# Kernel tuning notes

Measured on AMD Instinct MI355X. Metric: run time of the kernel, lower is better.

## Reference

```python
import jax, jax.numpy as jnp
import numpy as np

B, T, N = 32, 512, 16
C, V, D, H, L = 150, 832, 512, 512, 5  # chord vocab, note vocab, embed dim, hidden, layers


def setup_inputs() -> dict:
    key = jax.random.key(0)
    ks = jax.random.split(key, 16)
    s = 0.05
    note = jax.random.randint(ks[0], (B, T, N), 0, V)
    chord = jax.random.randint(ks[1], (B, T), 0, C)
    chord_table = jax.random.normal(ks[2], (C, D), jnp.float32) * s
    note_table = jax.random.normal(ks[3], (V, D), jnp.float32) * s
    # GRU layer 0 (input = 2*D), layers 1..L-1 (input = H), gate order r,z,n like torch
    w_ih0 = jax.random.normal(ks[4], (3 * H, 2 * D), jnp.float32) * s
    w_hh0 = jax.random.normal(ks[5], (3 * H, H), jnp.float32) * s
    b_ih0 = jax.random.normal(ks[6], (3 * H,), jnp.float32) * s
    b_hh0 = jax.random.normal(ks[7], (3 * H,), jnp.float32) * s
    w_ih_r = jax.random.normal(ks[8], (L - 1, 3 * H, H), jnp.float32) * s
    w_hh_r = jax.random.normal(ks[9], (L - 1, 3 * H, H), jnp.float32) * s
    b_ih_r = jax.random.normal(ks[10], (L - 1, 3 * H), jnp.float32) * s
    b_hh_r = jax.random.normal(ks[11], (L - 1, 3 * H), jnp.float32) * s
    fc_w = jax.random.normal(ks[12], (C, H), jnp.float32) * s
    fc_b = jax.random.normal(ks[13], (C,), jnp.float32) * s
    return dict(note=note, chord=chord, chord_table=chord_table, note_table=note_table,
                w_ih0=w_ih0, w_hh0=w_hh0, b_ih0=b_ih0, b_hh0=b_hh0,
                w_ih_r=w_ih_r, w_hh_r=w_hh_r, b_ih_r=b_ih_r, b_hh_r=b_hh_r,
                fc_w=fc_w, fc_b=fc_b)


def _gru_layer(x, wih, whh, bih, bhh):
    # x: [B, T, in] -> [B, T, H], torch GRU cell math (gate order r,z,n)
    xp = jnp.einsum('bti,gi->btg', x, wih) + bih          # precompute input proj [B,T,3H]
    xp = jnp.swapaxes(xp, 0, 1)                            # [T,B,3H]
    h0 = jnp.zeros((x.shape[0], whh.shape[1]), x.dtype)

    def step(h, xpt):
        gh = h @ whh.T + bhh
        xr, xz, xn = jnp.split(xpt, 3, axis=-1)
        hr, hz, hn = jnp.split(gh, 3, axis=-1)
        r = jax.nn.sigmoid(xr + hr)
        z = jax.nn.sigmoid(xz + hz)
        n = jnp.tanh(xn + r * hn)
        h_new = (1.0 - z) * n + z * h
        return h_new, h_new

    _, ys = jax.lax.scan(step, h0, xp)
    return jnp.swapaxes(ys, 0, 1)                          # [B,T,H]


def _forward(note, chord, chord_table, note_table, w_ih0, w_hh0, b_ih0, b_hh0,
             w_ih_r, w_hh_r, b_ih_r, b_hh_r, fc_w, fc_b):
    # padding_idx=0: zero row 0 of both tables (also blocks its gradient)
    ct = chord_table.at[0].set(0.0)
    nt = note_table.at[0].set(0.0)
    chord_emb = ct[chord]                                   # [B,T,D]
    # ragged mean over notes before first zero; mask[k]=1 iff no zero in note[...,:k+1]
    mask = jnp.cumprod((note != 0).astype(chord_table.dtype), axis=-1)  # [B,T,N]
    emb = nt[note]                                          # [B,T,N,D]
    cnt = jnp.maximum(mask.sum(-1), 1.0)                    # zero_index==0 case -> mean of zero row
    note_emb = jnp.einsum('btnd,btn->btd', emb, mask) / cnt[..., None]
    x = jnp.concatenate([chord_emb, note_emb], axis=-1)     # [B,T,2D]
    x = _gru_layer(x, w_ih0, w_hh0, b_ih0, b_hh0)
    for l in range(w_ih_r.shape[0]):
        x = _gru_layer(x, w_ih_r[l], w_hh_r[l], b_ih_r[l], b_hh_r[l])
    return x @ fc_w.T + fc_b                                # [B,T,C]


def reference(note, chord, chord_table, note_table, w_ih0, w_hh0, b_ih0, b_hh0,
              w_ih_r, w_hh_r, b_ih_r, b_hh_r, fc_w, fc_b):
    return _forward(note, chord, chord_table, note_table, w_ih0, w_hh0, b_ih0, b_hh0,
                    w_ih_r, w_hh_r, b_ih_r, b_hh_r, fc_w, fc_b)
```

## Files before the change

kernel.cpp:

```cpp
#include <hip/hip_runtime.h>
#include <hip/hip_bf16.h>

#define B_   32
#define T_   512
#define NN_  16
#define CV_  150
#define D_   512
#define H_   512
#define BT_  16384
#define K0_  1024
#define G3H_ 1536
#define SUBS_ 32
#define NBF_ 160
#define WSZ_ 49152

using bf16x8 = __attribute__((ext_vector_type(8))) short;
using f32x4  = __attribute__((ext_vector_type(4))) float;
using u32x4  = __attribute__((ext_vector_type(4))) unsigned int;
typedef unsigned long long u64;

__device__ __forceinline__ unsigned short f2bf(float f){
  unsigned int u = __builtin_bit_cast(unsigned int, f);
  u += 0x7fffu + ((u >> 16) & 1u);
  return (unsigned short)(u >> 16);
}

__device__ __forceinline__ void store8(unsigned short* p, f32x4 a, f32x4 b){
  union { unsigned short us[8]; u32x4 v; } u;
  u.us[0]=f2bf(a[0]); u.us[1]=f2bf(a[1]); u.us[2]=f2bf(a[2]); u.us[3]=f2bf(a[3]);
  u.us[4]=f2bf(b[0]); u.us[5]=f2bf(b[1]); u.us[6]=f2bf(b[2]); u.us[7]=f2bf(b[3]);
  *(u32x4*)p = u.v;
}

__device__ __forceinline__ u64 ld_coh_u64(const u64* p){
  return __hip_atomic_load(p, __ATOMIC_RELAXED, __HIP_MEMORY_SCOPE_AGENT);
}
__device__ __forceinline__ void st_coh_u32(void* p, unsigned int v){
  __hip_atomic_store((unsigned int*)p, v, __ATOMIC_RELAXED, __HIP_MEMORY_SCOPE_AGENT);
}
__device__ __forceinline__ void st_flag(int* p, int v){
  __hip_atomic_store(p, v, __ATOMIC_RELAXED, __HIP_MEMORY_SCOPE_AGENT);
}
__device__ __forceinline__ int ld_flag(const int* p){
  return __hip_atomic_load(p, __ATOMIC_RELAXED, __HIP_MEMORY_SCOPE_AGENT);
}

__global__ void convert_bf16(const float* __restrict__ src,
                             unsigned short* __restrict__ dst, int n){
  int i = blockIdx.x * 256 + threadIdx.x;
  if (i < n) dst[i] = f2bf(src[i]);
}

__global__ void prep_wfrag(const float* __restrict__ whh0,
                           const float* __restrict__ whhr,
                           const float* __restrict__ wihr,
                           unsigned short* __restrict__ wsw, int total){
  int idx = blockIdx.x * 256 + threadIdx.x;
  if (idx >= total) return;
  int pos = idx & 511;
  int lam = pos >> 3, e = pos & 7;
  int fr  = idx >> 9;
  int ks  = fr & 31;
  int g   = (fr >> 5) % 3;
  int blk = fr / 96;
  int sub = blk & 31, l = blk >> 5;
  int row = g * 512 + sub * 16 + (lam & 15);
  int k   = (ks & 15) * 32 + (lam >> 4) * 8 + e;
  float v;
  if (l == 0) v = (ks < 16) ? whh0[(size_t)row * H_ + k] : 0.f;
  else {
    const float* w = (ks < 16) ? (whhr + (size_t)(l - 1) * G3H_ * H_)
                               : (wihr + (size_t)(l - 1) * G3H_ * H_);
    v = w[(size_t)row * H_ + k];
  }
  wsw[idx] = f2bf(v);
}

__global__ void prep_bias(const float* __restrict__ bhh0,
                          const float* __restrict__ bihr,
                          const float* __restrict__ bhhr,
                          float* __restrict__ bias_sw, int total){
  int idx = blockIdx.x * 256 + threadIdx.x;
  if (idx >= total) return;
  int q = idx & 3, u = (idx >> 2) & 15, sub = (idx >> 6) & 31, l = idx >> 11;
  int j = sub * 16 + u;
  float v;
  if (l == 0){
    v = (q == 0) ? bhh0[j] : (q == 1) ? bhh0[512 + j] : (q == 2) ? 0.f : bhh0[1024 + j];
  } else {
    const float* bi = bihr + (size_t)(l - 1) * G3H_;
    const float* bh = bhhr + (size_t)(l - 1) * G3H_;
    v = (q == 0) ? bi[j] + bh[j]
      : (q == 1) ? bi[512 + j] + bh[512 + j]
      : (q == 2) ? bi[1024 + j] : bh[1024 + j];
  }
  bias_sw[idx] = v;
}

__global__ __launch_bounds__(64) void emb_kernel(
    const int* __restrict__ note, const int* __restrict__ chord,
    const float* __restrict__ ctab, const float* __restrict__ ntab,
    unsigned short* __restrict__ x0){
  const int bt = blockIdx.x;
  const int tid = threadIdx.x;
  __shared__ int sn[NN_];
  if (tid < NN_) sn[tid] = note[bt * NN_ + tid];
  __syncthreads();
  float alive = 1.f, cnt = 0.f;
  float msk[NN_];
  #pragma unroll
  for (int k = 0; k < NN_; ++k){ if (sn[k] == 0) alive = 0.f; msk[k] = alive; cnt += alive; }
  const float inv = 1.f / fmaxf(cnt, 1.f);
  const int ch = chord[bt];
  const int d0 = tid * 8;
  f32x4 c0 = {0.f,0.f,0.f,0.f}, c1 = {0.f,0.f,0.f,0.f};
  if (ch != 0){
    const float* cp = ctab + (size_t)ch * D_ + d0;
    c0 = *(const f32x4*)cp; c1 = *(const f32x4*)(cp + 4);
  }
  f32x4 s0 = {0.f,0.f,0.f,0.f}, s1 = {0.f,0.f,0.f,0.f};
  #pragma unroll
  for (int k = 0; k < NN_; ++k){
    if (msk[k] != 0.f){
      const float* np = ntab + (size_t)sn[k] * D_ + d0;
      s0 += *(const f32x4*)np;
      s1 += *(const f32x4*)(np + 4);
    }
  }
  s0 *= inv; s1 *= inv;
  unsigned short* o = x0 + (size_t)bt * K0_ + d0;
  store8(o, c0, c1);
  store8(o + D_, s0, s1);
}

__global__ __launch_bounds__(256) void gemm_bt(
    const unsigned short* __restrict__ X, const unsigned short* __restrict__ W,
    const float* __restrict__ bias, float* __restrict__ Y,
    int M, int N, int K, int wmode){
  const int lane = threadIdx.x & 63;
  const int wave = threadIdx.x >> 6;
  const int l15 = lane & 15, kq4 = lane >> 4;
  const int m_frag = blockIdx.y * 64 + wave * 16 + l15;
  const int n_base = blockIdx.x * 64;
  f32x4 acc[4] = {{0.f,0.f,0.f,0.f},{0.f,0.f,0.f,0.f},{0.f,0.f,0.f,0.f},{0.f,0.f,0.f,0.f}};
  const unsigned short* xptr = X + (size_t)m_frag * K + kq4 * 8;
  const unsigned short* wptr[4];
  #pragma unroll
  for (int i = 0; i < 4; ++i){
    int n = n_base + i * 16 + l15;
    if (n >= N) n = N - 1;
    wptr[i] = W + (size_t)n * K + kq4 * 8;
  }
  for (int k0 = 0; k0 < K; k0 += 32){
    bf16x8 a = *(const bf16x8*)(xptr + k0);
    #pragma unroll
    for (int i = 0; i < 4; ++i){
      bf16x8 b = *(const bf16x8*)(wptr[i] + k0);
      acc[i] = __builtin_amdgcn_mfma_f32_16x16x32_bf16(a, b, acc[i], 0, 0, 0);
    }
  }
  const int mrow = blockIdx.y * 64 + wave * 16 + kq4 * 4;
  #pragma unroll
  for (int i = 0; i < 4; ++i){
    int n = n_base + i * 16 + l15;
    if (n < N){
      float bv = bias[n];
      #pragma unroll
      for (int r = 0; r < 4; ++r){
        int m = mrow + r;
        float v = acc[i][r] + bv;
        if (wmode == 0) Y[(size_t)m * N + n] = v;
        else            Y[((size_t)(m & (T_-1)) * N + n) * B_ + (m >> 9)] = v;
      }
    }
  }
}

__global__ __launch_bounds__(256, 1) void gru_fused(
    const float* __restrict__ xp, const unsigned short* __restrict__ wsw,
    const float* __restrict__ bias_sw, unsigned short* __restrict__ hT,
    unsigned short* __restrict__ xT, unsigned short* __restrict__ xout,
    int* __restrict__ flags){
  __shared__ unsigned short w_s[96 * 512];
  __shared__ unsigned short stage_s[32 * 512];
  __shared__ float p_s[4][2][16][16];

  const int tid = threadIdx.x;
  const int blk = blockIdx.x;
  const int l   = blk >> 5;
  const int sub = blk & 31;
  const int lane = tid & 63, wave = tid >> 6;
  const int l15 = lane & 15, l4 = lane >> 4;
  const int myn = wave >> 1;
  const bool rzw = (wave & 1) == 0;

  {
    const u32x4* src = (const u32x4*)(wsw + (size_t)blk * WSZ_);
    u32x4* dst = (u32x4*)w_s;
    #pragma unroll
    for (int i = 0; i < 24; ++i) dst[tid + 256 * i] = src[tid + 256 * i];
  }

  const int cb = tid & 31;
  const int cj = (tid >> 5) * 2;
  const int jg = sub * 16 + cj;
  const float* bsp = bias_sw + blk * 64;
  const float br0 = bsp[cj*4+0],     bz0 = bsp[cj*4+1],     bx0 = bsp[cj*4+2],     bn0 = bsp[cj*4+3];
  const float br1 = bsp[(cj+1)*4+0], bz1 = bsp[(cj+1)*4+1], bx1 = bsp[(cj+1)*4+2], bn1 = bsp[(cj+1)*4+3];
  float hres0 = 0.f, hres1 = 0.f;

  unsigned short* hTl = hT + (size_t)l * (2 * 32 * 512);
  unsigned short* xTw = xT + (size_t)l * (4 * 32 * 512);
  const unsigned short* xTr = xT + (size_t)(l - 1) * (4 * 32 * 512);
  int*       fl_own  = flags + l * 64;
  const int* fl_prod = flags + (l > 0 ? (l - 1) * 64 : l * 64);
  const int* fl_cons = flags + (l + 1) * 64;

  __syncthreads();

  for (int t = 0; t < T_; ++t){
    if (wave == 0){
      const int* pp; int tgt;
      if (lane < 32){ pp = fl_own + lane; tgt = t; }
      else if (l > 0){ pp = fl_prod + (lane - 32); tgt = t + 1; }
      else { pp = fl_own + (lane - 32); tgt = -(1 << 30); }
      while (true){ int v = ld_flag(pp); if (__all(v >= tgt)) break; }
    } else if (wave == 1 && l < 4){
      const int* pp = fl_cons + (lane & 31);
      const int tgt = t - 3;
      while (true){
        int v = (lane < 32) ? ld_flag(pp) : 0x7fffffff;
        if (__all(v >= tgt)) break;
      }
    }
    __syncthreads();

    float er = 0.f, ez = 0.f, en = 0.f, er1 = 0.f, ez1 = 0.f, en1 = 0.f;
    if (l == 0){
      const float* xb = xp + (size_t)t * (G3H_ * B_) + cb;
      er  = xb[(size_t)(0 * H_ + jg) * B_];  er1 = xb[(size_t)(0 * H_ + jg + 1) * B_];
      ez  = xb[(size_t)(1 * H_ + jg) * B_];  ez1 = xb[(size_t)(1 * H_ + jg + 1) * B_];
      en  = xb[(size_t)(2 * H_ + jg) * B_];  en1 = xb[(size_t)(2 * H_ + jg + 1) * B_];
    }

    {
      const unsigned short* hsrc = hTl + (size_t)(t & 1) * (32 * 512);
      u64 lo[8], hi[8];
      #pragma unroll
      for (int i = 0; i < 8; ++i){
        int c = tid + 256 * i;
        int f = c >> 6, lam = c & 63;
        int b = ((f >> 4) << 4) | (lam & 15);
        int k = ((f & 15) << 5) | ((lam >> 4) << 3);
        const u64* sp = (const u64*)(hsrc + b * 512 + k);
        lo[i] = ld_coh_u64(sp);
        hi[i] = ld_coh_u64(sp + 1);
      }
      #pragma unroll
      for (int i = 0; i < 8; ++i){
        int c = tid + 256 * i;
        *(u64*)&stage_s[c * 8]     = lo[i];
        *(u64*)&stage_s[c * 8 + 4] = hi[i];
      }
    }

    union Ufrag { u64 q[2]; bf16x8 v; };
    Ufrag xb[16];
    if (l > 0){
      const unsigned short* xs = xTr + (size_t)(t & 3) * (32 * 512)
                               + (size_t)(myn * 16 + l15) * 512 + l4 * 8;
      #pragma unroll
      for (int ks = 0; ks < 16; ++ks){
        const u64* sp = (const u64*)(xs + ks * 32);
        xb[ks].q[0] = ld_coh_u64(sp);
        xb[ks].q[1] = ld_coh_u64(sp + 1);
      }
    }
    __syncthreads();

    f32x4 accA = {0.f,0.f,0.f,0.f}, accB = {0.f,0.f,0.f,0.f};
    #pragma unroll
    for (int ks = 0; ks < 16; ++ks){
      bf16x8 b = *(const bf16x8*)&stage_s[((myn << 4) + ks) * 512 + lane * 8];
      if (rzw){
        bf16x8 a0 = *(const bf16x8*)&w_s[(0 * 32 + ks) * 512 + lane * 8];
        bf16x8 a1 = *(const bf16x8*)&w_s[(1 * 32 + ks) * 512 + lane * 8];
        accA = __builtin_amdgcn_mfma_f32_16x16x32_bf16(a0, b, accA, 0, 0, 0);
        accB = __builtin_amdgcn_mfma_f32_16x16x32_bf16(a1, b, accB, 0, 0, 0);
      } else {
        bf16x8 a2 = *(const bf16x8*)&w_s[(2 * 32 + ks) * 512 + lane * 8];
        accA = __builtin_amdgcn_mfma_f32_16x16x32_bf16(a2, b, accA, 0, 0, 0);
      }
    }
    if (l > 0){
      #pragma unroll
      for (int ks = 0; ks < 16; ++ks){
        bf16x8 b = xb[ks].v;
        if (rzw){
          bf16x8 a0 = *(const bf16x8*)&w_s[(0 * 32 + 16 + ks) * 512 + lane * 8];
          bf16x8 a1 = *(const bf16x8*)&w_s[(1 * 32 + 16 + ks) * 512 + lane * 8];
          accA = __builtin_amdgcn_mfma_f32_16x16x32_bf16(a0, b, accA, 0, 0, 0);
          accB = __builtin_amdgcn_mfma_f32_16x16x32_bf16(a1, b, accB, 0, 0, 0);
        } else {
          bf16x8 a2 = *(const bf16x8*)&w_s[(2 * 32 + 16 + ks) * 512 + lane * 8];
          accB = __builtin_amdgcn_mfma_f32_16x16x32_bf16(a2, b, accB, 0, 0, 0);
        }
      }
    }
    #pragma unroll
    for (int r = 0; r < 4; ++r){
      int u = l4 * 4 + r;
      if (rzw){ p_s[0][myn][u][l15] = accA[r]; p_s[1][myn][u][l15] = accB[r]; }
      else    { p_s[2][myn][u][l15] = accA[r]; p_s[3][myn][u][l15] = accB[r]; }
    }
    __syncthreads();

    {
      const int nt = cb >> 4, bc = cb & 15;
      float rp0 = p_s[0][nt][cj][bc],     rp1 = p_s[0][nt][cj + 1][bc];
      float zp0 = p_s[1][nt][cj][bc],     zp1 = p_s[1][nt][cj + 1][bc];
      float hp0 = p_s[2][nt][cj][bc],     hp1 = p_s[2][nt][cj + 1][bc];
      float xq0 = p_s[3][nt][cj][bc],     xq1 = p_s[3][nt][cj + 1][bc];
      float r0 = 1.f / (1.f + __expf(-(rp0 + er  + br0)));
      float r1 = 1.f / (1.f + __expf(-(rp1 + er1 + br1)));
      float z0 = 1.f / (1.f + __expf(-(zp0 + ez  + bz0)));
      float z1 = 1.f / (1.f + __expf(-(zp1 + ez1 + bz1)));
      float nx0 = (l > 0) ? (xq0 + bx0) : en;
      float nx1 = (l > 0) ? (xq1 + bx1) : en1;
      float e0 = __expf(2.f * (nx0 + r0 * (hp0 + bn0)));
      float e1 = __expf(2.f * (nx1 + r1 * (hp1 + bn1)));
      float n0 = (e0 - 1.f) / (e0 + 1.f);
      float n1 = (e1 - 1.f) / (e1 + 1.f);
      float h0 = (1.f - z0) * n0 + z0 * hres0; hres0 = h0;
      float h1 = (1.f - z1) * n1 + z1 * hres1; hres1 = h1;
      unsigned int pk = (unsigned int)f2bf(h0) | ((unsigned int)f2bf(h1) << 16);
      st_coh_u32(hTl + (size_t)((t + 1) & 1) * (32 * 512) + cb * 512 + jg, pk);
      if (l < 4) st_coh_u32(xTw + (size_t)(t & 3) * (32 * 512) + cb * 512 + jg, pk);
      else *(unsigned int*)&xout[((size_t)cb * T_ + t) * H_ + jg] = pk;
    }
    __syncthreads();
    if (tid == 0) st_flag(fl_own + sub, t + 1);
  }
}

extern "C" void kernel_launch(void* const* d_in, const int* in_sizes, int n_in,
                              void* d_out, int out_size, void* d_ws, size_t ws_size,
                              hipStream_t stream){
  (void)in_sizes; (void)n_in; (void)out_size; (void)ws_size;
  const int*   note  = (const int*)d_in[0];
  const int*   chord = (const int*)d_in[1];
  const float* ctab  = (const float*)d_in[2];
  const float* ntab  = (const float*)d_in[3];
  const float* wih0  = (const float*)d_in[4];
  const float* whh0  = (const float*)d_in[5];
  const float* bih0  = (const float*)d_in[6];
  const float* bhh0  = (const float*)d_in[7];
  const float* wihr  = (const float*)d_in[8];
  const float* whhr  = (const float*)d_in[9];
  const float* bihr  = (const float*)d_in[10];
  const float* bhhr  = (const float*)d_in[11];
  const float* fcw   = (const float*)d_in[12];
  const float* fcb   = (const float*)d_in[13];
  float* out = (float*)d_out;

  char* ws = (char*)d_ws;
  size_t off = 0;
  auto alloc = [&](size_t bytes)->char*{
    char* p = ws + off; off = (off + bytes + 255) & ~(size_t)255; return p;
  };
  int*            flags   = (int*)alloc((size_t)5 * 64 * sizeof(int));
  float*          xp      = (float*)alloc((size_t)BT_ * G3H_ * 4);
  unsigned short* x0      = (unsigned short*)alloc((size_t)BT_ * K0_ * 2);
  unsigned short* xout    = (unsigned short*)alloc((size_t)BT_ * H_ * 2);
  unsigned short* hT      = (unsigned short*)alloc((size_t)5 * 2 * 32 * 512 * 2);
  unsigned short* xT      = (unsigned short*)alloc((size_t)4 * 4 * 32 * 512 * 2);
  unsigned short* wsw     = (unsigned short*)alloc((size_t)NBF_ * WSZ_ * 2);
  float*          bias_sw = (float*)alloc((size_t)NBF_ * 64 * 4);
  unsigned short* wih0_b  = (unsigned short*)alloc((size_t)G3H_ * K0_ * 2);
  unsigned short* fcw_b   = (unsigned short*)alloc((size_t)CV_ * H_ * 2);

  hipMemsetAsync(flags, 0, (size_t)5 * 64 * sizeof(int), stream);
  hipMemsetAsync(hT, 0, (size_t)5 * 2 * 32 * 512 * 2, stream);

  { int n = G3H_ * K0_; convert_bf16<<<(n + 255) / 256, 256, 0, stream>>>(wih0, wih0_b, n); }
  { int n = CV_ * H_;   convert_bf16<<<(n + 255) / 256, 256, 0, stream>>>(fcw, fcw_b, n); }
  { int n = NBF_ * WSZ_;
    prep_wfrag<<<(n + 255) / 256, 256, 0, stream>>>(whh0, whhr, wihr, wsw, n); }
  { int n = NBF_ * 64;
    prep_bias<<<(n + 255) / 256, 256, 0, stream>>>(bhh0, bihr, bhhr, bias_sw, n); }

  emb_kernel<<<BT_, 64, 0, stream>>>(note, chord, ctab, ntab, x0);

  gemm_bt<<<dim3(G3H_ / 64, BT_ / 64), 256, 0, stream>>>(x0, wih0_b, bih0, xp, BT_, G3H_, K0_, 1);

  gru_fused<<<NBF_, 256, 0, stream>>>(xp, wsw, bias_sw, hT, xT, xout, flags);

  gemm_bt<<<dim3((CV_ + 63) / 64, BT_ / 64), 256, 0, stream>>>(
      xout, fcw_b, fcb, out, BT_, CV_, H_, 0);
}
```

Baseline: 6.090 ms.

## Tag hidden-state words with step counters to replace flag barriers in fused GRU

Each bf16 hidden/input value is now stored with a 16-bit timestep tag, so consumers poll the data itself rather than waiting on per-block producer flags before reading. The own-layer flag wait is loosened to a slack of two steps, buffers become four-deep, and the end-of-step barrier is removed. The layer-input fragments are staged through padded shared memory instead of registers. This aims to cut cross-block flag round-trips and barriers on the sequential recurrence critical path, at the cost of doubled buffer traffic, spin loops with sleeps, and extra syncthreads around the input staging.

```diff
diff --git a/kernel.cpp b/kernel.cpp
--- a/kernel.cpp
+++ b/kernel.cpp
@@ -13,6 +13,7 @@
 #define SUBS_ 32
 #define NBF_ 160
 #define WSZ_ 49152
+#define FS_  520
 
 using bf16x8 = __attribute__((ext_vector_type(8))) short;
 using f32x4  = __attribute__((ext_vector_type(4))) float;
@@ -35,8 +36,8 @@
 __device__ __forceinline__ u64 ld_coh_u64(const u64* p){
   return __hip_atomic_load(p, __ATOMIC_RELAXED, __HIP_MEMORY_SCOPE_AGENT);
 }
-__device__ __forceinline__ void st_coh_u32(void* p, unsigned int v){
-  __hip_atomic_store((unsigned int*)p, v, __ATOMIC_RELAXED, __HIP_MEMORY_SCOPE_AGENT);
+__device__ __forceinline__ void st_coh_u64s(u64* p, u64 v){
+  __hip_atomic_store(p, v, __ATOMIC_RELAXED, __HIP_MEMORY_SCOPE_AGENT);
 }
 __device__ __forceinline__ void st_flag(int* p, int v){
   __hip_atomic_store(p, v, __ATOMIC_RELAXED, __HIP_MEMORY_SCOPE_AGENT);
@@ -178,11 +179,11 @@
 
 __global__ __launch_bounds__(256, 1) void gru_fused(
     const float* __restrict__ xp, const unsigned short* __restrict__ wsw,
-    const float* __restrict__ bias_sw, unsigned short* __restrict__ hT,
-    unsigned short* __restrict__ xT, unsigned short* __restrict__ xout,
+    const float* __restrict__ bias_sw, unsigned int* __restrict__ hT,
+    unsigned int* __restrict__ xT, unsigned short* __restrict__ xout,
     int* __restrict__ flags){
   __shared__ unsigned short w_s[96 * 512];
-  __shared__ unsigned short stage_s[32 * 512];
+  __shared__ unsigned short stage_s[32 * FS_];
   __shared__ float p_s[4][2][16][16];
 
   const int tid = threadIdx.x;
@@ -209,31 +210,70 @@
   const float br1 = bsp[(cj+1)*4+0], bz1 = bsp[(cj+1)*4+1], bx1 = bsp[(cj+1)*4+2], bn1 = bsp[(cj+1)*4+3];
   float hres0 = 0.f, hres1 = 0.f;
 
-  unsigned short* hTl = hT + (size_t)l * (2 * 32 * 512);
-  unsigned short* xTw = xT + (size_t)l * (4 * 32 * 512);
-  const unsigned short* xTr = xT + (size_t)(l - 1) * (4 * 32 * 512);
+  unsigned int* hTl = hT + (size_t)l * (4 * 32 * 512);
+  unsigned int* xTw = xT + (size_t)l * (4 * 32 * 512);
+  const unsigned int* xTr = xT + (size_t)(l - 1) * (4 * 32 * 512);
   int*       fl_own  = flags + l * 64;
-  const int* fl_prod = flags + (l > 0 ? (l - 1) * 64 : l * 64);
-  const int* fl_cons = flags + (l + 1) * 64;
+  const int* fl_cons = flags + (l < 4 ? (l + 1) * 64 : l * 64);
+
+  st_coh_u64s((u64*)&hTl[(size_t)cb * 512 + jg], 0x0000000100000001ull);
+
+  const int bl_ = tid & 15;
+  const int qh_ = ((tid >> 4) & 15) * 4;
+  const int wv_ = tid >> 6;
+  const int lanef_ = ((tid >> 4) & 3) * 16 + (tid & 15);
+
+  auto issue32 = [&](const u64* sbase, u64 (&v)[8][4]){
+    #pragma unroll
+    for (int i = 0; i < 8; ++i){
+      const u64* sp = sbase + ((size_t)(bl_ | ((i & 1) << 4)) << 8) + qh_ + ((i >> 1) << 6);
+      #pragma unroll
+      for (int j = 0; j < 4; ++j) v[i][j] = ld_coh_u64(sp + j);
+    }
+  };
+  auto finish32 = [&](const u64* sbase, u64 (&v)[8][4], u64 wantp){
+    while (true){
+      unsigned bad = 0;
+      #pragma unroll
+      for (int i = 0; i < 8; ++i)
+        #pragma unroll
+        for (int j = 0; j < 4; ++j)
+          if ((v[i][j] & 0x0000FFFF0000FFFFull) != wantp) bad |= 1u << (i * 4 + j);
+      if (!bad) break;
+      __builtin_amdgcn_s_sleep(1);
+      #pragma unroll
+      for (int i = 0; i < 8; ++i){
+        const u64* sp = sbase + ((size_t)(bl_ | ((i & 1) << 4)) << 8) + qh_ + ((i >> 1) << 6);
+        #pragma unroll
+        for (int j = 0; j < 4; ++j)
+          if ((bad >> (i * 4 + j)) & 1) v[i][j] = ld_coh_u64(sp + j);
+      }
+    }
+    #pragma unroll
+    for (int i = 0; i < 8; ++i){
+      int f = ((i & 1) << 4) + ((i >> 1) << 2) + wv_;
+      u32x4 o;
+      #pragma unroll
+      for (int j = 0; j < 4; ++j)
+        o[j] = (unsigned)((v[i][j] >> 16) & 0xFFFFu)
+             | (unsigned)((v[i][j] >> 32) & 0xFFFF0000u);
+      *(u32x4*)&stage_s[(size_t)f * FS_ + (size_t)lanef_ * 8] = o;
+    }
+  };
 
   __syncthreads();
 
   for (int t = 0; t < T_; ++t){
     if (wave == 0){
       const int* pp; int tgt;
-      if (lane < 32){ pp = fl_own + lane; tgt = t; }
-      else if (l > 0){ pp = fl_prod + (lane - 32); tgt = t + 1; }
-      else { pp = fl_own + (lane - 32); tgt = -(1 << 30); }
-      while (true){ int v = ld_flag(pp); if (__all(v >= tgt)) break; }
-    } else if (wave == 1 && l < 4){
-      const int* pp = fl_cons + (lane & 31);
-      const int tgt = t - 3;
-      while (true){
-        int v = (lane < 32) ? ld_flag(pp) : 0x7fffffff;
-        if (__all(v >= tgt)) break;
-      }
-    }
-    __syncthreads();
+      if (lane < 32){ pp = fl_own + lane; tgt = t - 2; }
+      else { pp = fl_cons + (lane - 32); tgt = (l < 4) ? (t - 3) : (-(1 << 30)); }
+      int vv = ld_flag(pp);
+      while (!__all(vv >= tgt)){ __builtin_amdgcn_s_sleep(1); vv = ld_flag(pp); }
+    }
+
+    const unsigned want = (unsigned)(t + 1);
+    const u64 wantp = (u64)want | ((u64)want << 32);
 
     float er = 0.f, ez = 0.f, en = 0.f, er1 = 0.f, ez1 = 0.f, en1 = 0.f;
     if (l == 0){
@@ -243,45 +283,19 @@
       en  = xb[(size_t)(2 * H_ + jg) * B_];  en1 = xb[(size_t)(2 * H_ + jg + 1) * B_];
     }
 
-    {
-      const unsigned short* hsrc = hTl + (size_t)(t & 1) * (32 * 512);
-      u64 lo[8], hi[8];
-      #pragma unroll
-      for (int i = 0; i < 8; ++i){
-        int c = tid + 256 * i;
-        int f = c >> 6, lam = c & 63;
-        int b = ((f >> 4) << 4) | (lam & 15);
-        int k = ((f & 15) << 5) | ((lam >> 4) << 3);
-        const u64* sp = (const u64*)(hsrc + b * 512 + k);
-        lo[i] = ld_coh_u64(sp);
-        hi[i] = ld_coh_u64(sp + 1);
-      }
-      #pragma unroll
-      for (int i = 0; i < 8; ++i){
-        int c = tid + 256 * i;
-        *(u64*)&stage_s[c * 8]     = lo[i];
-        *(u64*)&stage_s[c * 8 + 4] = hi[i];
-      }
-    }
-
-    union Ufrag { u64 q[2]; bf16x8 v; };
-    Ufrag xb[16];
-    if (l > 0){
-      const unsigned short* xs = xTr + (size_t)(t & 3) * (32 * 512)
-                               + (size_t)(myn * 16 + l15) * 512 + l4 * 8;
-      #pragma unroll
-      for (int ks = 0; ks < 16; ++ks){
-        const u64* sp = (const u64*)(xs + ks * 32);
-        xb[ks].q[0] = ld_coh_u64(sp);
-        xb[ks].q[1] = ld_coh_u64(sp + 1);
-      }
-    }
+    const u64* hbase = (const u64*)(hTl + (size_t)(t & 3) * (32 * 512));
+    u64 vh[8][4], vx[8][4];
+    issue32(hbase, vh);
+    finish32(hbase, vh, wantp);
     __syncthreads();
 
+    const u64* xbase = (const u64*)(xTr + (size_t)(t & 3) * (32 * 512));
+    if (l > 0) issue32(xbase, vx);
+
     f32x4 accA = {0.f,0.f,0.f,0.f}, accB = {0.f,0.f,0.f,0.f};
     #pragma unroll
     for (int ks = 0; ks < 16; ++ks){
-      bf16x8 b = *(const bf16x8*)&stage_s[((myn << 4) + ks) * 512 + lane * 8];
+      bf16x8 b = *(const bf16x8*)&stage_s[(size_t)((myn << 4) + ks) * FS_ + lane * 8];
       if (rzw){
         bf16x8 a0 = *(const bf16x8*)&w_s[(0 * 32 + ks) * 512 + lane * 8];
         bf16x8 a1 = *(const bf16x8*)&w_s[(1 * 32 + ks) * 512 + lane * 8];
@@ -293,9 +307,12 @@
       }
     }
     if (l > 0){
+      __syncthreads();
+      finish32(xbase, vx, wantp);
+      __syncthreads();
       #pragma unroll
       for (int ks = 0; ks < 16; ++ks){
-        bf16x8 b = xb[ks].v;
+        bf16x8 b = *(const bf16x8*)&stage_s[(size_t)((myn << 4) + ks) * FS_ + lane * 8];
         if (rzw){
           bf16x8 a0 = *(const bf16x8*)&w_s[(0 * 32 + 16 + ks) * 512 + lane * 8];
           bf16x8 a1 = *(const bf16x8*)&w_s[(1 * 32 + 16 + ks) * 512 + lane * 8];
@@ -307,6 +324,8 @@
         }
       }
     }
+    if (tid == 0) st_flag(fl_own + sub, t + 1);
+
     #pragma unroll
     for (int r = 0; r < 4; ++r){
       int u = l4 * 4 + r;
@@ -333,13 +352,18 @@
       float n1 = (e1 - 1.f) / (e1 + 1.f);
       float h0 = (1.f - z0) * n0 + z0 * hres0; hres0 = h0;
       float h1 = (1.f - z1) * n1 + z1 * hres1; hres1 = h1;
-      unsigned int pk = (unsigned int)f2bf(h0) | ((unsigned int)f2bf(h1) << 16);
-      st_coh_u32(hTl + (size_t)((t + 1) & 1) * (32 * 512) + cb * 512 + jg, pk);
-      if (l < 4) st_coh_u32(xTw + (size_t)(t & 3) * (32 * 512) + cb * 512 + jg, pk);
-      else *(unsigned int*)&xout[((size_t)cb * T_ + t) * H_ + jg] = pk;
-    }
-    __syncthreads();
-    if (tid == 0) st_flag(fl_own + sub, t + 1);
+      unsigned hb0 = f2bf(h0), hb1 = f2bf(h1);
+      u64 hv = ((u64)((hb1 << 16) | (unsigned)(t + 2)) << 32)
+             |  (u64)((hb0 << 16) | (unsigned)(t + 2));
+      st_coh_u64s((u64*)&hTl[(size_t)((t + 1) & 3) * (32 * 512) + cb * 512 + jg], hv);
+      if (l < 4){
+        u64 xv = ((u64)((hb1 << 16) | want) << 32)
+               |  (u64)((hb0 << 16) | want);
+        st_coh_u64s((u64*)&xTw[(size_t)(t & 3) * (32 * 512) + cb * 512 + jg], xv);
+      } else {
+        *(unsigned int*)&xout[((size_t)cb * T_ + t) * H_ + jg] = hb0 | (hb1 << 16);
+      }
+    }
   }
 }
 
@@ -372,15 +396,16 @@
   float*          xp      = (float*)alloc((size_t)BT_ * G3H_ * 4);
   unsigned short* x0      = (unsigned short*)alloc((size_t)BT_ * K0_ * 2);
   unsigned short* xout    = (unsigned short*)alloc((size_t)BT_ * H_ * 2);
-  unsigned short* hT      = (unsigned short*)alloc((size_t)5 * 2 * 32 * 512 * 2);
-  unsigned short* xT      = (unsigned short*)alloc((size_t)4 * 4 * 32 * 512 * 2);
+  unsigned int*   hT      = (unsigned int*)alloc((size_t)5 * 4 * 32 * 512 * 4);
+  unsigned int*   xT      = (unsigned int*)alloc((size_t)4 * 4 * 32 * 512 * 4);
   unsigned short* wsw     = (unsigned short*)alloc((size_t)NBF_ * WSZ_ * 2);
   float*          bias_sw = (float*)alloc((size_t)NBF_ * 64 * 4);
   unsigned short* wih0_b  = (unsigned short*)alloc((size_t)G3H_ * K0_ * 2);
   unsigned short* fcw_b   = (unsigned short*)alloc((size_t)CV_ * H_ * 2);
 
   hipMemsetAsync(flags, 0, (size_t)5 * 64 * sizeof(int), stream);
-  hipMemsetAsync(hT, 0, (size_t)5 * 2 * 32 * 512 * 2, stream);
+  hipMemsetAsync(hT, 0, (size_t)5 * 4 * 32 * 512 * 4, stream);
+  hipMemsetAsync(xT, 0, (size_t)4 * 4 * 32 * 512 * 4, stream);
 
   { int n = G3H_ * K0_; convert_bf16<<<(n + 255) / 256, 256, 0, stream>>>(wih0, wih0_b, n); }
   { int n = CV_ * H_;   convert_bf16<<<(n + 255) / 256, 256, 0, stream>>>(fcw, fcw_b, n); }
```

Result: slower. 7.708 ms (+26.6%).
